# Kernel optimization log

Measured on AMD Instinct MI355X. Metric: run time of the kernel, lower is better.

Reference implementation:

```python
import jax, jax.numpy as jnp
import numpy as np

B, S, D = 4, 2048, 1024
H, HD = 16, 64
TAU = HD ** -0.5
N_MASKED = 256  # last keys masked (padding)


def setup_inputs() -> dict:
    key = jax.random.key(0)
    ks = jax.random.split(key, 8)
    sc = 0.02
    mask = jnp.zeros((B, 1, 1, S), dtype=bool).at[..., S - N_MASKED:].set(True)
    return {
        "q": jax.random.normal(ks[0], (B, S, D), dtype=jnp.float32),
        "k": jax.random.normal(ks[1], (B, S, D), dtype=jnp.float32),
        "v": jax.random.normal(ks[2], (B, S, D), dtype=jnp.float32),
        "mask": mask,
        "Wq": jax.random.normal(ks[3], (D, H * HD), dtype=jnp.float32) * sc,
        "bq": jnp.zeros((H * HD,), dtype=jnp.float32),
        "Wk": jax.random.normal(ks[4], (D, H * HD), dtype=jnp.float32) * sc,
        "bk": jnp.zeros((H * HD,), dtype=jnp.float32),
        "Wv": jax.random.normal(ks[5], (D, H * HD), dtype=jnp.float32) * sc,
        "bv": jnp.zeros((H * HD,), dtype=jnp.float32),
        "Wo": jax.random.normal(ks[6], (H * HD, D), dtype=jnp.float32) * sc,
        "bo": jnp.zeros((D,), dtype=jnp.float32),
    }


def reference(q, k, v, mask, Wq, bq, Wk, bk, Wv, bv, Wo, bo):
    # projections: [..., s, D] -> [..., s, H, HD]
    qh = (q @ Wq + bq).reshape(*q.shape[:-1], H, HD)
    kh = (k @ Wk + bk).reshape(*k.shape[:-1], H, HD)
    vh = (v @ Wv + bv).reshape(*v.shape[:-1], H, HD)
    # scores: [B, H, Q, K]
    attn = jnp.einsum('bqhd,bkhd->bhqk', qh, kh) * TAU
    attn = jnp.where(mask, -jnp.inf, attn)  # masked_fill(mask, -inf)
    # dropout(p=0) before softmax is identity
    p = jax.nn.softmax(attn, axis=-1)
    out = jnp.einsum('bhqk,bkhd->bqhd', p, vh).reshape(*q.shape[:-1], H * HD)
    return out @ Wo + bo  # [B, S, D]
```

## Files before the change

### kernel.cpp

```cpp
#include <hip/hip_runtime.h>
#include <hip/hip_fp16.h>
#include <cstdint>
#include <cstddef>

#define B_  4
#define S_  2048
#define D_  1024
#define H_  16
#define HD_ 64
#define TAU_ 0.125f
#define QSCALE_ 0.18033688011112042f

typedef _Float16 f16;
typedef __attribute__((ext_vector_type(8)))  _Float16 f16x8;
typedef __attribute__((ext_vector_type(4)))  _Float16 f16x4;
typedef __attribute__((ext_vector_type(2)))  __fp16   fp16x2_b;
typedef __attribute__((ext_vector_type(4)))  float    f32x4;
typedef __attribute__((ext_vector_type(16))) float    f32x16;
typedef __attribute__((ext_vector_type(2)))  unsigned u32x2;

__device__ __forceinline__ void gload_lds16(const f16* g, f16* l) {
    __builtin_amdgcn_global_load_lds(
        (const __attribute__((address_space(1))) unsigned int*)g,
        (__attribute__((address_space(3)))       unsigned int*)l,
        16, 0, 0);
}

__device__ __forceinline__ unsigned pkh(float a, float b) {
    fp16x2_b h = __builtin_amdgcn_cvt_pkrtz(a, b);
    return __builtin_bit_cast(unsigned, h);
}

__device__ __forceinline__ float exp2_hw(float x) {
    float r;
    asm("v_exp_f32 %0, %1" : "=v"(r) : "v"(x));
    return r;
}

__device__ __forceinline__ float pair_max(float x) {
    unsigned xu = __builtin_bit_cast(unsigned, x);
    u32x2 r = __builtin_amdgcn_permlane32_swap(xu, xu, false, false);
    return fmaxf(__builtin_bit_cast(float, r[0]), __builtin_bit_cast(float, r[1]));
}
__device__ __forceinline__ float pair_sum(float x) {
    unsigned xu = __builtin_bit_cast(unsigned, x);
    u32x2 r = __builtin_amdgcn_permlane32_swap(xu, xu, false, false);
    return __builtin_bit_cast(float, r[0]) + __builtin_bit_cast(float, r[1]);
}

__global__ __launch_bounds__(256) void mask_norm_kernel(
    const unsigned char* __restrict__ mp, unsigned char* __restrict__ nm,
    float* __restrict__ mf)
{
    __shared__ int flags[3];
    const int tid = threadIdx.x;
    if (tid < 3) flags[tid] = 0;
    __syncthreads();
    int loc0 = 0, loc1 = 0, loc2 = 0;
    for (int i = 0; i < 32; ++i) {
        int off = tid * 32 + i;
        unsigned char v = mp[off];
        if (v) {
            int m = off & 3;
            if (m == 0) loc0 = 1;
            else if (m == 1) loc1 = 1;
            else loc2 = 1;
        }
    }
    if (loc0) atomicOr(&flags[0], 1);
    if (loc1) atomicOr(&flags[1], 1);
    if (loc2) atomicOr(&flags[2], 1);
    __syncthreads();
    const int mode = flags[1] ? 0 : (flags[2] ? 2 : (flags[0] ? 1 : 0));
    for (int i = 0; i < 32; ++i) {
        int idx = tid * 32 + i;
        unsigned char r;
        if (mode == 0)      r = mp[idx] ? 1 : 0;
        else if (mode == 1) r = ((const int*)mp)[idx] ? 1 : 0;
        else                r = (((const float*)mp)[idx] != 0.f) ? 1 : 0;
        nm[idx] = r;
        mf[idx] = r ? -1e30f : 0.f;
    }
}

__global__ __launch_bounds__(256) void wconv_kernel(
    const float* __restrict__ W0, const float* __restrict__ W1,
    const float* __restrict__ W2, const float* __restrict__ W3,
    f16* __restrict__ Wt)
{
    __shared__ float T[64][65];
    const int z = blockIdx.z;
    const float* W = (z == 0) ? W0 : (z == 1) ? W1 : (z == 2) ? W2 : W3;
    f16* out = Wt + (size_t)z * D_ * D_;
    const int n0 = blockIdx.x * 64, k0 = blockIdx.y * 64;
    const int tid = threadIdx.x;
    for (int j = 0; j < 4; ++j) {
        int idx = j * 256 + tid;
        int r = idx >> 4, c4 = idx & 15;
        float4 v = *(const float4*)&W[(size_t)(k0 + r) * D_ + n0 + c4 * 4];
        T[r][c4 * 4 + 0] = v.x; T[r][c4 * 4 + 1] = v.y;
        T[r][c4 * 4 + 2] = v.z; T[r][c4 * 4 + 3] = v.w;
    }
    __syncthreads();
    for (int j = 0; j < 16; ++j) {
        int idx = j * 256 + tid;
        int nl = idx >> 6, kl = idx & 63;
        out[(size_t)(n0 + nl) * D_ + k0 + kl] = (f16)T[kl][nl];
    }
}

__global__ __launch_bounds__(256) void f32to16_kernel(
    const float* __restrict__ a0, const float* __restrict__ a1,
    const float* __restrict__ a2, f16* __restrict__ o0,
    f16* __restrict__ o1, f16* __restrict__ o2)
{
    const int z = blockIdx.y;
    const float* a = (z == 0) ? a0 : (z == 1) ? a1 : a2;
    f16* o = (z == 0) ? o0 : (z == 1) ? o1 : o2;
    const int N4 = (B_ * S_ * D_) / 4;
    for (int i = blockIdx.x * 256 + threadIdx.x; i < N4; i += gridDim.x * 256) {
        float4 v = ((const float4*)a)[i];
        f16x4 h;
        h[0] = (f16)v.x; h[1] = (f16)v.y; h[2] = (f16)v.z; h[3] = (f16)v.w;
        ((f16x4*)o)[i] = h;
    }
}

template <bool A16>
__device__ __forceinline__ void gemm_body(
    const void* __restrict__ Ap, const f16* __restrict__ Wt,
    const float* __restrict__ bias, void* __restrict__ Cp,
    int m0, int n0, float oscale, int outmode)
{
    __shared__ __align__(16) f16 Al[128 * 64];
    __shared__ __align__(16) f16 Bl[128 * 64];
    const int tid = threadIdx.x, lane = tid & 63, wid = tid >> 6;
    const int wm = (wid >> 1) * 64, wn = (wid & 1) * 64;
    const int g = lane >> 4, c = lane & 15;

    f32x4 acc[4][4] = {};

    for (int kt = 0; kt < 16; ++kt) {
        const int k0 = kt * 64;
        for (int i = 0; i < 4; ++i) {
            int ch  = wid * 4 + i;
            int row = ch * 8 + (lane >> 3);
            int ls  = (lane & 7) ^ (row & 7);
            gload_lds16(Wt + (size_t)(n0 + row) * 1024 + k0 + ls * 8,
                        Bl + ch * 512);
        }
        if (A16) {
            const f16* A = (const f16*)Ap;
            for (int i = 0; i < 4; ++i) {
                int ch  = wid * 4 + i;
                int row = ch * 8 + (lane >> 3);
                int ls  = (lane & 7) ^ (row & 7);
                gload_lds16(A + (size_t)(m0 + row) * 1024 + k0 + ls * 8,
                            Al + ch * 512);
            }
        } else {
            const float* A = (const float*)Ap;
            for (int j = 0; j < 8; ++j) {
                int idx = j * 256 + tid;
                int row = idx >> 4, c4 = idx & 15;
                float4 v = *(const float4*)&A[(size_t)(m0 + row) * 1024 + k0 + c4 * 4];
                f16x4 h;
                h[0] = (f16)v.x; h[1] = (f16)v.y; h[2] = (f16)v.z; h[3] = (f16)v.w;
                int ps = (c4 >> 1) ^ (row & 7);
                *(f16x4*)&Al[row * 64 + ps * 8 + (c4 & 1) * 4] = h;
            }
        }
        __syncthreads();
        for (int kc = 0; kc < 2; ++kc) {
            f16x8 af[4], bf[4];
            for (int mb = 0; mb < 4; ++mb) {
                int row = wm + mb * 16 + c;
                af[mb] = *(const f16x8*)&Al[row * 64 + ((kc * 4 + g) ^ (row & 7)) * 8];
            }
            for (int nb = 0; nb < 4; ++nb) {
                int row = wn + nb * 16 + c;
                bf[nb] = *(const f16x8*)&Bl[row * 64 + ((kc * 4 + g) ^ (row & 7)) * 8];
            }
            for (int mb = 0; mb < 4; ++mb)
                for (int nb = 0; nb < 4; ++nb)
                    acc[mb][nb] = __builtin_amdgcn_mfma_f32_16x16x32_f16(
                        af[mb], bf[nb], acc[mb][nb], 0, 0, 0);
        }
        __syncthreads();
    }
    for (int nb = 0; nb < 4; ++nb) {
        int n = n0 + wn + nb * 16 + c;
        float bv = bias[n];
        for (int mb = 0; mb < 4; ++mb)
            for (int r = 0; r < 4; ++r) {
                int m = m0 + wm + mb * 16 + g * 4 + r;
                float v = (acc[mb][nb][r] + bv) * oscale;
                if (outmode == 1) {
                    ((f16*)Cp)[(((size_t)(m >> 11) * H_ + (n >> 6)) * HD_ + (n & 63)) * S_ + (m & 2047)] = (f16)v;
                } else if (outmode == 0) {
                    ((f16*)Cp)[(size_t)m * 1024 + n] = (f16)v;
                } else {
                    ((float*)Cp)[(size_t)m * 1024 + n] = v;
                }
            }
    }
}

__global__ __launch_bounds__(256) void gemm_qkv16_kernel(
    const f16* __restrict__ qf, const f16* __restrict__ kf,
    const f16* __restrict__ vf, const f16* __restrict__ Wt,
    const float* __restrict__ bq, const float* __restrict__ bk,
    const float* __restrict__ bv, f16* __restrict__ outbase)
{
    const int z = blockIdx.z;
    const f16* A    = (z == 0) ? qf : (z == 1) ? kf : vf;
    const float* bi = (z == 0) ? bq : (z == 1) ? bk : bv;
    gemm_body<true>(A, Wt + (size_t)z * D_ * D_, bi,
                    outbase + (size_t)z * S_ * B_ * D_,
                    blockIdx.x * 128, blockIdx.y * 128,
                    z == 0 ? QSCALE_ : 1.f, z == 2 ? 1 : 0);
}

__global__ __launch_bounds__(256) void gemm_qkv32_kernel(
    const float* __restrict__ q, const float* __restrict__ k,
    const float* __restrict__ v, const f16* __restrict__ Wt,
    const float* __restrict__ bq, const float* __restrict__ bk,
    const float* __restrict__ bv, f16* __restrict__ outbase)
{
    const int z = blockIdx.z;
    const float* A  = (z == 0) ? q  : (z == 1) ? k  : v;
    const float* bi = (z == 0) ? bq : (z == 1) ? bk : bv;
    gemm_body<false>(A, Wt + (size_t)z * D_ * D_, bi,
                     outbase + (size_t)z * S_ * B_ * D_,
                     blockIdx.x * 128, blockIdx.y * 128,
                     z == 0 ? QSCALE_ : 1.f, z == 2 ? 1 : 0);
}

__global__ __launch_bounds__(256) void gemm_out_kernel(
    const f16* __restrict__ Oh, const f16* __restrict__ WtO,
    const float* __restrict__ bo, float* __restrict__ out)
{
    gemm_body<true>(Oh, WtO, bo, out, blockIdx.x * 128, blockIdx.y * 128, 1.f, 2);
}

__global__ __launch_bounds__(256) void attn_kernel(
    const f16* __restrict__ qh, const f16* __restrict__ kh,
    const f16* __restrict__ vt, const unsigned char* __restrict__ maskp,
    const float* __restrict__ maskf, f16* __restrict__ Oh)
{
    __shared__ __align__(16) f16 Kl[2][64 * 64];
    __shared__ __align__(16) f16 VTl[2][64 * 64];
    const int tid = threadIdx.x, lane = tid & 63, wid = tid >> 6;
    const int ql = lane & 31, hi = lane >> 5;
    const int lg = ((blockIdx.x & 7) << 7) + (blockIdx.x >> 3);
    const int h = (lg >> 4) & 15, b = lg >> 8;
    const int q0 = (lg & 15) * 128 + wid * 32;

    const unsigned char* mrow = maskp + (size_t)b * S_;
    const float* mfrow = maskf + (size_t)b * S_;
    const size_t kbase  = (size_t)b * S_ * D_ + (size_t)h * HD_;
    const size_t vtbase = ((size_t)b * H_ + h) * (size_t)HD_ * S_;

    unsigned live = 0, part = 0;
    for (int t = 0; t < 32; ++t) {
        unsigned long long bal = __ballot(mrow[t * 64 + lane] != 0);
        if (bal != ~0ull) {
            live |= 1u << t;
            if (bal) part |= 1u << t;
        }
    }

    f16x8 qf[4];
    {
        const f16* qrow = qh + ((size_t)(b * S_ + q0 + ql) * H_ + h) * HD_;
        #pragma unroll
        for (int dc = 0; dc < 4; ++dc)
            qf[dc] = *(const f16x8*)&qrow[dc * 16 + hi * 8];
    }

    float m_ = -1e30f, l_ = 0.f;
    f32x16 accO[2] = {};

    auto stage = [&](int kv0, int bb) {
        #pragma unroll
        for (int i = 0; i < 2; ++i) {
            int ch  = wid * 2 + i;
            int row = ch * 8 + (lane >> 3);
            int ls  = (lane & 7) ^ (row & 7);
            gload_lds16(kh + kbase + (size_t)(kv0 + row) * D_ + ls * 8,
                        &Kl[bb][ch * 512]);
            gload_lds16(vt + vtbase + (size_t)row * S_ + kv0 + ls * 8,
                        &VTl[bb][ch * 512]);
        }
    };

    if (live) {
        int t = __builtin_ctz(live);
        stage(t * 64, 0);
        __syncthreads();
        int cur = 0;
        for (;;) {
            unsigned rem = live & (0xFFFFFFFEu << t);
            int tn = rem ? __builtin_ctz(rem) : 32;
            if (tn < 32) stage(tn * 64, cur ^ 1);

            const int kv0 = t * 64;
            const f16* Kb = &Kl[cur][0];
            const f16* Vb = &VTl[cur][0];

            f32x16 sacc[2] = {};
            #pragma unroll
            for (int ks = 0; ks < 2; ++ks) {
                const int key = ks * 32 + ql;
                #pragma unroll
                for (int dc = 0; dc < 4; ++dc) {
                    int slot = (dc * 2 + hi) ^ (key & 7);
                    f16x8 kf = *(const f16x8*)&Kb[key * 64 + slot * 8];
                    sacc[ks] = __builtin_amdgcn_mfma_f32_32x32x16_f16(
                        kf, qf[dc], sacc[ks], 0, 0, 0);
                }
            }
            if (part & (1u << t)) {
                #pragma unroll
                for (int ks = 0; ks < 2; ++ks)
                    #pragma unroll
                    for (int r = 0; r < 16; ++r) {
                        int key = kv0 + ks * 32 + (r & 3) + 8 * (r >> 2) + 4 * hi;
                        sacc[ks][r] += mfrow[key];
                    }
            }
            float mx = sacc[0][0];
            #pragma unroll
            for (int ks = 0; ks < 2; ++ks)
                #pragma unroll
                for (int r = 0; r < 16; ++r) mx = fmaxf(mx, sacc[ks][r]);
            mx = pair_max(mx);
            if (__ballot(mx > m_ + 8.f)) {
                float mnew = fmaxf(m_, mx);
                float alpha = exp2_hw(m_ - mnew);
                m_ = mnew;
                l_ *= alpha;
                #pragma unroll
                for (int blk = 0; blk < 2; ++blk)
                    #pragma unroll
                    for (int r = 0; r < 16; ++r) accO[blk][r] *= alpha;
            }
            float ts = 0.f;
            #pragma unroll
            for (int ks = 0; ks < 2; ++ks)
                #pragma unroll
                for (int r = 0; r < 16; ++r) {
                    float p = exp2_hw(sacc[ks][r] - m_);
                    sacc[ks][r] = p;
                    ts += p;
                }
            l_ += pair_sum(ts);

            #pragma unroll
            for (int ks = 0; ks < 2; ++ks) {
                unsigned Pq[4][2];
                #pragma unroll
                for (int j = 0; j < 4; ++j) {
                    Pq[j][0] = pkh(sacc[ks][4 * j + 0], sacc[ks][4 * j + 1]);
                    Pq[j][1] = pkh(sacc[ks][4 * j + 2], sacc[ks][4 * j + 3]);
                }
                #pragma unroll
                for (int kc = 0; kc < 2; ++kc) {
                    union { f16x8 v; unsigned u[4]; } pf;
                    u32x2 s0 = __builtin_amdgcn_permlane32_swap(Pq[2 * kc][0], Pq[2 * kc + 1][0], false, false);
                    u32x2 s1 = __builtin_amdgcn_permlane32_swap(Pq[2 * kc][1], Pq[2 * kc + 1][1], false, false);
                    pf.u[0] = s0[0]; pf.u[2] = s0[1];
                    pf.u[1] = s1[0]; pf.u[3] = s1[1];
                    #pragma unroll
                    for (int blk = 0; blk < 2; ++blk) {
                        int hd = blk * 32 + ql;
                        int slot = (ks * 4 + kc * 2 + hi) ^ (hd & 7);
                        f16x8 vtf = *(const f16x8*)&Vb[hd * 64 + slot * 8];
                        accO[blk] = __builtin_amdgcn_mfma_f32_32x32x16_f16(
                            vtf, pf.v, accO[blk], 0, 0, 0);
                    }
                }
            }
            __syncthreads();
            cur ^= 1;
            if (tn == 32) break;
            t = tn;
        }
    }
    const float invl = (l_ > 0.f) ? 1.f / l_ : 0.f;
    f16* orow = Oh + ((size_t)(b * S_ + q0 + ql) * H_ + h) * HD_;
    #pragma unroll
    for (int blk = 0; blk < 2; ++blk)
        #pragma unroll
        for (int j = 0; j < 4; ++j) {
            f16x4 o;
            #pragma unroll
            for (int tt = 0; tt < 4; ++tt)
                o[tt] = (f16)(accO[blk][4 * j + tt] * invl);
            *(f16x4*)&orow[blk * 32 + 4 * hi + 8 * j] = o;
        }
}

extern "C" void kernel_launch(void* const* d_in, const int* in_sizes, int n_in,
                              void* d_out, int out_size, void* d_ws, size_t ws_size,
                              hipStream_t stream)
{
    const float* q    = (const float*)d_in[0];
    const float* k    = (const float*)d_in[1];
    const float* v    = (const float*)d_in[2];
    const unsigned char* mask = (const unsigned char*)d_in[3];
    const float* Wq   = (const float*)d_in[4];
    const float* bq   = (const float*)d_in[5];
    const float* Wk   = (const float*)d_in[6];
    const float* bk   = (const float*)d_in[7];
    const float* Wv   = (const float*)d_in[8];
    const float* bv   = (const float*)d_in[9];
    const float* Wo   = (const float*)d_in[10];
    const float* bo   = (const float*)d_in[11];
    float* out        = (float*)d_out;

    char* ws = (char*)d_ws;
    const size_t MB = 1048576;
    f16* Wt  = (f16*)ws;
    f16* qh  = (f16*)(ws + 8 * MB);
    f16* khp = (f16*)(ws + 24 * MB);
    f16* vtp = (f16*)(ws + 40 * MB);
    f16* Ohp = (f16*)(ws + 56 * MB);
    unsigned char* nm = (unsigned char*)(ws + 72 * MB);
    float* mf = (float*)(ws + 72 * MB + 8192);
    f16* qf16 = (f16*)(ws + 76 * MB);
    f16* kf16 = (f16*)(ws + 92 * MB);
    f16* vf16 = (f16*)(ws + 108 * MB);
    const bool use16 = ws_size >= 124 * MB;

    mask_norm_kernel<<<1, 256, 0, stream>>>(mask, nm, mf);
    wconv_kernel<<<dim3(16, 16, 4), 256, 0, stream>>>(Wq, Wk, Wv, Wo, Wt);
    if (use16) {
        f32to16_kernel<<<dim3(1024, 3), 256, 0, stream>>>(q, k, v, qf16, kf16, vf16);
        gemm_qkv16_kernel<<<dim3(64, 8, 3), 256, 0, stream>>>(
            qf16, kf16, vf16, Wt, bq, bk, bv, qh);
    } else {
        gemm_qkv32_kernel<<<dim3(64, 8, 3), 256, 0, stream>>>(
            q, k, v, Wt, bq, bk, bv, qh);
    }
    attn_kernel<<<1024, 256, 0, stream>>>(qh, khp, vtp, nm, mf, Ohp);
    gemm_out_kernel<<<dim3(64, 8), 256, 0, stream>>>(Ohp, Wt + (size_t)3 * D_ * D_, bo, out);
}
```

Before: 256.8 us.

## Double the attention KV tile to 128 keys with new V swizzle and setprio

Enlarges the attention kernel's key/value tile from 64 to 128 keys per iteration. This halves the number of barriers and softmax-rescale checks, and each tile now does more MFMA work. The mask liveness scan, LDS staging and V-transpose XOR swizzle are adjusted to the wider rows. It also wraps the MFMA loops in s_setprio, uses v_max3 for the row max, and sets launch bounds to 2 blocks per CU. LDS use doubles (64 KB per block), and the larger score arrays raise register pressure, which may cost occupancy.

```diff
diff --git a/kernel.cpp b/kernel.cpp
--- a/kernel.cpp
+++ b/kernel.cpp
@@ -34,6 +34,12 @@
 __device__ __forceinline__ float exp2_hw(float x) {
     float r;
     asm("v_exp_f32 %0, %1" : "=v"(r) : "v"(x));
+    return r;
+}
+
+__device__ __forceinline__ float max3f(float a, float b, float c) {
+    float r;
+    asm("v_max3_f32 %0, %1, %2, %3" : "=v"(r) : "v"(a), "v"(b), "v"(c));
     return r;
 }
 
@@ -243,13 +249,13 @@
     gemm_body<true>(Oh, WtO, bo, out, blockIdx.x * 128, blockIdx.y * 128, 1.f, 2);
 }
 
-__global__ __launch_bounds__(256) void attn_kernel(
+__global__ __launch_bounds__(256, 2) void attn_kernel(
     const f16* __restrict__ qh, const f16* __restrict__ kh,
     const f16* __restrict__ vt, const unsigned char* __restrict__ maskp,
     const float* __restrict__ maskf, f16* __restrict__ Oh)
 {
-    __shared__ __align__(16) f16 Kl[2][64 * 64];
-    __shared__ __align__(16) f16 VTl[2][64 * 64];
+    __shared__ __align__(16) f16 Kl[2][128 * 64];
+    __shared__ __align__(16) f16 VTl[2][64 * 128];
     const int tid = threadIdx.x, lane = tid & 63, wid = tid >> 6;
     const int ql = lane & 31, hi = lane >> 5;
     const int lg = ((blockIdx.x & 7) << 7) + (blockIdx.x >> 3);
@@ -262,11 +268,12 @@
     const size_t vtbase = ((size_t)b * H_ + h) * (size_t)HD_ * S_;
 
     unsigned live = 0, part = 0;
-    for (int t = 0; t < 32; ++t) {
-        unsigned long long bal = __ballot(mrow[t * 64 + lane] != 0);
-        if (bal != ~0ull) {
+    for (int t = 0; t < 16; ++t) {
+        unsigned long long b0 = __ballot(mrow[t * 128 + lane] != 0);
+        unsigned long long b1 = __ballot(mrow[t * 128 + 64 + lane] != 0);
+        if (b0 != ~0ull || b1 != ~0ull) {
             live |= 1u << t;
-            if (bal) part |= 1u << t;
+            if (b0 | b1) part |= 1u << t;
         }
     }
 
@@ -283,34 +290,37 @@
 
     auto stage = [&](int kv0, int bb) {
         #pragma unroll
-        for (int i = 0; i < 2; ++i) {
-            int ch  = wid * 2 + i;
+        for (int i = 0; i < 4; ++i) {
+            int ch  = wid * 4 + i;
             int row = ch * 8 + (lane >> 3);
             int ls  = (lane & 7) ^ (row & 7);
             gload_lds16(kh + kbase + (size_t)(kv0 + row) * D_ + ls * 8,
                         &Kl[bb][ch * 512]);
-            gload_lds16(vt + vtbase + (size_t)row * S_ + kv0 + ls * 8,
+            int hdr = ch * 4 + (lane >> 4);
+            int vs  = (lane & 15) ^ ((hdr & 7) << 1);
+            gload_lds16(vt + vtbase + (size_t)hdr * S_ + kv0 + vs * 8,
                         &VTl[bb][ch * 512]);
         }
     };
 
     if (live) {
         int t = __builtin_ctz(live);
-        stage(t * 64, 0);
+        stage(t * 128, 0);
         __syncthreads();
         int cur = 0;
         for (;;) {
             unsigned rem = live & (0xFFFFFFFEu << t);
             int tn = rem ? __builtin_ctz(rem) : 32;
-            if (tn < 32) stage(tn * 64, cur ^ 1);
-
-            const int kv0 = t * 64;
+            if (tn < 32) stage(tn * 128, cur ^ 1);
+
+            const int kv0 = t * 128;
             const f16* Kb = &Kl[cur][0];
             const f16* Vb = &VTl[cur][0];
 
-            f32x16 sacc[2] = {};
+            f32x16 sacc[4] = {};
+            __builtin_amdgcn_s_setprio(1);
             #pragma unroll
-            for (int ks = 0; ks < 2; ++ks) {
+            for (int ks = 0; ks < 4; ++ks) {
                 const int key = ks * 32 + ql;
                 #pragma unroll
                 for (int dc = 0; dc < 4; ++dc) {
@@ -320,20 +330,34 @@
                         kf, qf[dc], sacc[ks], 0, 0, 0);
                 }
             }
+            __builtin_amdgcn_s_setprio(0);
             if (part & (1u << t)) {
                 #pragma unroll
-                for (int ks = 0; ks < 2; ++ks)
+                for (int ks = 0; ks < 4; ++ks)
                     #pragma unroll
                     for (int r = 0; r < 16; ++r) {
                         int key = kv0 + ks * 32 + (r & 3) + 8 * (r >> 2) + 4 * hi;
                         sacc[ks][r] += mfrow[key];
                     }
             }
-            float mx = sacc[0][0];
-            #pragma unroll
-            for (int ks = 0; ks < 2; ++ks)
-                #pragma unroll
-                for (int r = 0; r < 16; ++r) mx = fmaxf(mx, sacc[ks][r]);
+            float mx;
+            {
+                float m0 = max3f(sacc[0][0], sacc[0][1], sacc[0][2]);
+                float m1 = max3f(sacc[1][0], sacc[1][1], sacc[1][2]);
+                float m2 = max3f(sacc[2][0], sacc[2][1], sacc[2][2]);
+                float m3 = max3f(sacc[3][0], sacc[3][1], sacc[3][2]);
+                #pragma unroll
+                for (int r = 3; r < 15; r += 2) {
+                    m0 = max3f(m0, sacc[0][r], sacc[0][r + 1]);
+                    m1 = max3f(m1, sacc[1][r], sacc[1][r + 1]);
+                    m2 = max3f(m2, sacc[2][r], sacc[2][r + 1]);
+                    m3 = max3f(m3, sacc[3][r], sacc[3][r + 1]);
+                }
+                m0 = fmaxf(m0, sacc[0][15]); m1 = fmaxf(m1, sacc[1][15]);
+                m2 = fmaxf(m2, sacc[2][15]); m3 = fmaxf(m3, sacc[3][15]);
+                mx = max3f(m0, m1, m2);
+                mx = fmaxf(mx, m3);
+            }
             mx = pair_max(mx);
             if (__ballot(mx > m_ + 8.f)) {
                 float mnew = fmaxf(m_, mx);
@@ -347,7 +371,7 @@
             }
             float ts = 0.f;
             #pragma unroll
-            for (int ks = 0; ks < 2; ++ks)
+            for (int ks = 0; ks < 4; ++ks)
                 #pragma unroll
                 for (int r = 0; r < 16; ++r) {
                     float p = exp2_hw(sacc[ks][r] - m_);
@@ -357,7 +381,7 @@
             l_ += pair_sum(ts);
 
             #pragma unroll
-            for (int ks = 0; ks < 2; ++ks) {
+            for (int ks = 0; ks < 4; ++ks) {
                 unsigned Pq[4][2];
                 #pragma unroll
                 for (int j = 0; j < 4; ++j) {
@@ -371,14 +395,17 @@
                     u32x2 s1 = __builtin_amdgcn_permlane32_swap(Pq[2 * kc][1], Pq[2 * kc + 1][1], false, false);
                     pf.u[0] = s0[0]; pf.u[2] = s0[1];
                     pf.u[1] = s1[0]; pf.u[3] = s1[1];
+                    const int s = ks * 2 + kc;
+                    __builtin_amdgcn_s_setprio(1);
                     #pragma unroll
                     for (int blk = 0; blk < 2; ++blk) {
                         int hd = blk * 32 + ql;
-                        int slot = (ks * 4 + kc * 2 + hi) ^ (hd & 7);
-                        f16x8 vtf = *(const f16x8*)&Vb[hd * 64 + slot * 8];
+                        int slot = (s * 2 + hi) ^ ((hd & 7) << 1);
+                        f16x8 vtf = *(const f16x8*)&Vb[hd * 128 + slot * 8];
                         accO[blk] = __builtin_amdgcn_mfma_f32_32x32x16_f16(
                             vtf, pf.v, accO[blk], 0, 0, 0);
                     }
+                    __builtin_amdgcn_s_setprio(0);
                 }
             }
             __syncthreads();
```

New measurement: 243.5 us. -5.2%, faster.
